# Performance work log

Measured on AMD Instinct MI355X. Metric: run time of the kernel, lower is better.

Reference implementation:

```python
import jax, jax.numpy as jnp
import numpy as np

N_NODES = 40000
N_EDGES = 640000
NFEAT = 256
NHID = 128


def setup_inputs() -> dict:
    key = jax.random.key(0)
    k1, k2, k3, k4 = jax.random.split(key, 4)
    x = jax.random.normal(k1, (N_NODES, NFEAT), dtype=jnp.float32)
    edge_index = jax.random.randint(k2, (2, N_EDGES), 0, N_NODES, dtype=jnp.int64)
    edge_weight = jax.random.uniform(k3, (N_EDGES,), dtype=jnp.float32)
    # Glorot-style init for the GraphConvolution weight, zero bias
    W = jax.random.normal(k4, (NFEAT, NHID), dtype=jnp.float32) * (1.0 / np.sqrt(NFEAT))
    b = jnp.zeros((NHID,), dtype=jnp.float32)
    return {"x": x, "edge_index": edge_index, "edge_weight": edge_weight, "W": W, "b": b}


def reference(x, edge_index, edge_weight, W, b):
    # GraphConvolution: support = x @ W ; out = spmm(adj, support) + b ; relu
    support = x @ W                                   # [N, nhid]
    src, dst = edge_index[0], edge_index[1]
    msgs = support[src] * edge_weight[:, None]        # [E, nhid] gathered messages
    agg = jax.ops.segment_sum(msgs, dst, num_segments=N_NODES)  # [N, nhid]
    return jax.nn.relu(agg + b)
```

## Files before the change

kernel.cpp:

```cpp
#include <hip/hip_runtime.h>

#define NNODES 40000
#define NEDGES 640000
#define NFEAT  256
#define NHID   128

#define RSHIFT 7
#define RNODES 128
#define NR     313
#define PARTB  250
#define EPT    10
#define EPB    2560
#define CAPB   32
#define GEMM_BLOCKS (NNODES / 64)
#define WSPLIT 4
#define WNODES 32
#define CAPW   1024

#define SUP_OFF  0u
#define WT_OFF   10240000u
#define CNT_OFF  10305536u
#define EBIN_OFF 10465536u
#define WS_NEEDED (EBIN_OFF + (size_t)NR * PARTB * CAPB * 8)

typedef float floatx4 __attribute__((ext_vector_type(4)));
typedef __bf16 bf16x8 __attribute__((ext_vector_type(8)));
typedef unsigned short ushort8 __attribute__((ext_vector_type(8)));
union BfFrag { ushort8 s; bf16x8 b; };

__device__ __forceinline__ unsigned short f2bf(float f) {
    unsigned int u = __float_as_uint(f);
    u = (u + 0x7FFFu + ((u >> 16) & 1u)) >> 16;
    return (unsigned short)u;
}

__device__ __forceinline__ float4 bf4(unsigned int lo, unsigned int hi) {
    float4 v;
    v.x = __uint_as_float(lo << 16);
    v.y = __uint_as_float(lo & 0xFFFF0000u);
    v.z = __uint_as_float(hi << 16);
    v.w = __uint_as_float(hi & 0xFFFF0000u);
    return v;
}

__global__ __launch_bounds__(256) void setup_wt(const float* __restrict__ W,
                                                unsigned short* __restrict__ Wt) {
    const int i = blockIdx.x * 256 + threadIdx.x;
    const int h = i >> 8;
    const int k = i & 255;
    Wt[i] = f2bf(W[k * NHID + h]);
}

__global__ __launch_bounds__(256) void gemm_fill(const float* __restrict__ x,
                                                 const unsigned short* __restrict__ Wt,
                                                 unsigned short* __restrict__ support,
                                                 const int* __restrict__ ei,
                                                 const float* __restrict__ ew,
                                                 unsigned short* __restrict__ cnt,
                                                 unsigned long long* __restrict__ ebin) {
    const int tid = threadIdx.x;

    if (blockIdx.x >= GEMM_BLOCKS) {
        __shared__ unsigned int ldscur[320];
        const int pb   = blockIdx.x - GEMM_BLOCKS;
        const int base = pb * EPB + tid;

        for (int i = tid; i < 320; i += 256) ldscur[i] = 0u;
        __syncthreads();

        int src[EPT], dst[EPT];
        float w[EPT];
        #pragma unroll
        for (int j = 0; j < EPT; j++) {
            const int e = base + j * 256;
            src[j] = ei[e];
            dst[j] = ei[NEDGES + e];
            w[j]   = ew[e];
        }
        #pragma unroll
        for (int j = 0; j < EPT; j++) {
            const int r = dst[j] >> RSHIFT;
            const unsigned int idx = atomicAdd(&ldscur[r], 1u);
            if (idx < CAPB) {
                const unsigned long long rec =
                    ((unsigned long long)f2bf(w[j]) << 32)
                  | ((unsigned long long)(dst[j] & (RNODES - 1)) << 16)
                  | (unsigned long long)(unsigned int)src[j];
                ebin[((size_t)r * PARTB + pb) * CAPB + idx] = rec;
            }
        }
        __syncthreads();

        for (int i = tid; i < NR; i += 256) {
            unsigned int c = ldscur[i];
            if (c > CAPB) c = CAPB;
            cnt[(size_t)pb * NR + i] = (unsigned short)c;
        }
        return;
    }

    const int lane = tid & 63;
    const int wv   = tid >> 6;
    const int m    = lane & 15;
    const int quad = lane >> 4;
    const int node = blockIdx.x * 64 + wv * 16 + m;

    BfFrag afrag[8];
    const float* xrow = x + (size_t)node * NFEAT + quad * 8;
    #pragma unroll
    for (int ks = 0; ks < 8; ks++) {
        float4 f0 = *(const float4*)(xrow + ks * 32);
        float4 f1 = *(const float4*)(xrow + ks * 32 + 4);
        afrag[ks].s[0] = f2bf(f0.x); afrag[ks].s[1] = f2bf(f0.y);
        afrag[ks].s[2] = f2bf(f0.z); afrag[ks].s[3] = f2bf(f0.w);
        afrag[ks].s[4] = f2bf(f1.x); afrag[ks].s[5] = f2bf(f1.y);
        afrag[ks].s[6] = f2bf(f1.z); afrag[ks].s[7] = f2bf(f1.w);
    }

    floatx4 acc[8];
    #pragma unroll
    for (int nt = 0; nt < 8; nt++) acc[nt] = (floatx4){0.f, 0.f, 0.f, 0.f};

    #pragma unroll
    for (int nt = 0; nt < 8; nt++) {
        const unsigned short* wrow = Wt + (size_t)(nt * 16 + m) * NFEAT + quad * 8;
        #pragma unroll
        for (int ks = 0; ks < 8; ks++) {
            BfFrag bfrag;
            bfrag.s = *(const ushort8*)(wrow + ks * 32);
            acc[nt] = __builtin_amdgcn_mfma_f32_16x16x32_bf16(afrag[ks].b, bfrag.b,
                                                              acc[nt], 0, 0, 0);
        }
    }

    const int row0 = blockIdx.x * 64 + wv * 16 + quad * 4;
    #pragma unroll
    for (int nt = 0; nt < 8; nt++) {
        #pragma unroll
        for (int r = 0; r < 4; r++) {
            support[(size_t)(row0 + r) * NHID + nt * 16 + m] = f2bf(acc[nt][r]);
        }
    }
}

__global__ __launch_bounds__(512) void gather_range(
        const unsigned short* __restrict__ cnt,
        const unsigned long long* __restrict__ ebin,
        const unsigned short* __restrict__ support,
        const float* __restrict__ b,
        float* __restrict__ out) {
    __shared__ unsigned long long srec[CAPW];
    __shared__ unsigned int hcnt[WNODES];
    __shared__ unsigned int hstart[WNODES + 1];
    __shared__ unsigned int sA[WNODES], sB[WNODES];

    const int r   = blockIdx.x >> 2;
    const int q   = blockIdx.x & 3;
    const int tid = threadIdx.x;

    unsigned int c_t = 0;
    const unsigned long long* seg =
        ebin + ((size_t)r * PARTB + (tid < PARTB ? tid : 0)) * CAPB;
    if (tid < PARTB) {
        c_t = cnt[(size_t)tid * NR + r];
        if (c_t > CAPB) c_t = CAPB;
    }
    if (tid < WNODES) hcnt[tid] = 0u;
    __syncthreads();

    for (unsigned int k = 0; k < c_t; ++k) {
        const unsigned int dl = (unsigned int)(seg[k] >> 16) & (RNODES - 1);
        if ((int)(dl >> 5) == q) atomicAdd(&hcnt[dl & (WNODES - 1)], 1u);
    }
    __syncthreads();

    if (tid < WNODES) sA[tid] = (tid > 0) ? hcnt[tid - 1] : 0u;
    __syncthreads();
    unsigned int* cur = sA;
    unsigned int* nxt = sB;
    for (int off = 1; off < WNODES; off <<= 1) {
        if (tid < WNODES) nxt[tid] = cur[tid] + ((tid >= off) ? cur[tid - off] : 0u);
        __syncthreads();
        unsigned int* t = cur; cur = nxt; nxt = t;
    }
    if (tid < WNODES) hstart[tid] = cur[tid];
    if (tid == WNODES - 1) hstart[WNODES] = cur[WNODES - 1] + hcnt[WNODES - 1];
    __syncthreads();
    if (tid < WNODES) hcnt[tid] = hstart[tid];
    __syncthreads();

    for (unsigned int k = 0; k < c_t; ++k) {
        const unsigned long long rec = seg[k];
        const unsigned int dl = (unsigned int)(rec >> 16) & (RNODES - 1);
        if ((int)(dl >> 5) == q) {
            const unsigned int p = atomicAdd(&hcnt[dl & (WNODES - 1)], 1u);
            if (p < CAPW) srec[p] = rec;
        }
    }
    __syncthreads();

    const int nl = tid >> 4;
    const int ql = tid & 15;
    unsigned int kb = hstart[nl];
    unsigned int ke = hstart[nl + 1];
    if (kb > CAPW) kb = CAPW;
    if (ke > CAPW) ke = CAPW;

    float4 lo = make_float4(0.f, 0.f, 0.f, 0.f);
    float4 hi = lo;
    const uint4* sup4 = (const uint4*)support;

    #pragma unroll 2
    for (unsigned int k = kb; k < ke; ++k) {
        const unsigned long long rec = srec[k];
        const float w  = __uint_as_float(((unsigned int)(rec >> 32)) << 16);
        const int   sc = (int)(rec & 0xFFFFu);
        const uint4 u  = sup4[(size_t)sc * 16 + ql];
        const float4 vl = bf4(u.x, u.y), vh = bf4(u.z, u.w);
        lo.x = fmaf(w, vl.x, lo.x); lo.y = fmaf(w, vl.y, lo.y);
        lo.z = fmaf(w, vl.z, lo.z); lo.w = fmaf(w, vl.w, lo.w);
        hi.x = fmaf(w, vh.x, hi.x); hi.y = fmaf(w, vh.y, hi.y);
        hi.z = fmaf(w, vh.z, hi.z); hi.w = fmaf(w, vh.w, hi.w);
    }

    const int node = r * RNODES + q * WNODES + nl;
    if (node < NNODES) {
        const float4* b4p = (const float4*)b;
        float4 bl = b4p[ql * 2], bh = b4p[ql * 2 + 1];
        lo.x = fmaxf(lo.x + bl.x, 0.f); lo.y = fmaxf(lo.y + bl.y, 0.f);
        lo.z = fmaxf(lo.z + bl.z, 0.f); lo.w = fmaxf(lo.w + bl.w, 0.f);
        hi.x = fmaxf(hi.x + bh.x, 0.f); hi.y = fmaxf(hi.y + bh.y, 0.f);
        hi.z = fmaxf(hi.z + bh.z, 0.f); hi.w = fmaxf(hi.w + bh.w, 0.f);
        float4* o4 = (float4*)out + (size_t)node * (NHID / 4);
        o4[ql * 2]     = lo;
        o4[ql * 2 + 1] = hi;
    }
}

__global__ __launch_bounds__(256) void gemm_xw(const float* __restrict__ x,
                                               const float* __restrict__ W,
                                               float* __restrict__ support) {
    __shared__ float xs[64 * NFEAT];
    const int tid   = threadIdx.x;
    const int node0 = blockIdx.x * 64;

    const float4* xg  = (const float4*)(x + (size_t)node0 * NFEAT);
    float4*       xs4 = (float4*)xs;
    #pragma unroll
    for (int i = tid; i < 64 * (NFEAT / 4); i += 256) xs4[i] = xg[i];
    __syncthreads();

    const int hg = tid & 31;
    const int ng = tid >> 5;
    const float4* W4 = (const float4*)W;

    float4 acc[8];
    #pragma unroll
    for (int n = 0; n < 8; n++) acc[n] = make_float4(0.f, 0.f, 0.f, 0.f);

    #pragma unroll 4
    for (int k = 0; k < NFEAT; k++) {
        float4 w = W4[k * (NHID / 4) + hg];
        #pragma unroll
        for (int n = 0; n < 8; n++) {
            float xv = xs[(ng * 8 + n) * NFEAT + k];
            acc[n].x = fmaf(xv, w.x, acc[n].x);
            acc[n].y = fmaf(xv, w.y, acc[n].y);
            acc[n].z = fmaf(xv, w.z, acc[n].z);
            acc[n].w = fmaf(xv, w.w, acc[n].w);
        }
    }

    float4* out4 = (float4*)support;
    #pragma unroll
    for (int n = 0; n < 8; n++)
        out4[(size_t)(node0 + ng * 8 + n) * (NHID / 4) + hg] = acc[n];
}

__global__ __launch_bounds__(256) void scatter_edges(const int* __restrict__ ei,
                                                     const float* __restrict__ ew,
                                                     const float* __restrict__ support,
                                                     float* __restrict__ out) {
    const int tid  = threadIdx.x;
    const int lane = tid & 31;
    const int e    = blockIdx.x * 8 + (tid >> 5);
    const int   src = ei[e];
    const int   dst = ei[NEDGES + e];
    const float w   = ew[e];
    const float4* s4 = (const float4*)support;
    float4 v = s4[(size_t)src * (NHID / 4) + lane];
    float* o = out + (size_t)dst * NHID + lane * 4;
    atomicAdd(o + 0, v.x * w);
    atomicAdd(o + 1, v.y * w);
    atomicAdd(o + 2, v.z * w);
    atomicAdd(o + 3, v.w * w);
}

__global__ __launch_bounds__(256) void finalize(float* __restrict__ out,
                                                const float* __restrict__ b) {
    const int i = blockIdx.x * 256 + threadIdx.x;
    float4*       o4 = (float4*)out;
    const float4* b4 = (const float4*)b;
    float4 v  = o4[i];
    float4 bb = b4[i & 31];
    v.x = fmaxf(v.x + bb.x, 0.f);
    v.y = fmaxf(v.y + bb.y, 0.f);
    v.z = fmaxf(v.z + bb.z, 0.f);
    v.w = fmaxf(v.w + bb.w, 0.f);
    o4[i] = v;
}

extern "C" void kernel_launch(void* const* d_in, const int* in_sizes, int n_in,
                              void* d_out, int out_size, void* d_ws, size_t ws_size,
                              hipStream_t stream) {
    const float* x  = (const float*)d_in[0];
    const int*   ei = (const int*)d_in[1];
    const float* ew = (const float*)d_in[2];
    const float* W  = (const float*)d_in[3];
    const float* b  = (const float*)d_in[4];
    float*       out = (float*)d_out;

    char* ws = (char*)d_ws;

    if (ws_size >= WS_NEEDED) {
        unsigned short*     support = (unsigned short*)(ws + SUP_OFF);
        unsigned short*     Wt      = (unsigned short*)(ws + WT_OFF);
        unsigned short*     cnt     = (unsigned short*)(ws + CNT_OFF);
        unsigned long long* ebin    = (unsigned long long*)(ws + EBIN_OFF);

        setup_wt<<<128, 256, 0, stream>>>(W, Wt);
        gemm_fill<<<GEMM_BLOCKS + PARTB, 256, 0, stream>>>(
            x, Wt, support, ei, ew, cnt, ebin);
        gather_range<<<NR * WSPLIT, 512, 0, stream>>>(cnt, ebin, support, b, out);
    } else {
        float* support = (float*)(ws + SUP_OFF);
        gemm_xw<<<NNODES / 64, 256, 0, stream>>>(x, W, support);
        hipMemsetAsync(d_out, 0, (size_t)out_size * sizeof(float), stream);
        scatter_edges<<<NEDGES / 8, 256, 0, stream>>>(ei, ew, support, out);
        finalize<<<out_size / 4 / 256, 256, 0, stream>>>(out, b);
    }
}
```

Measured before the change: 168.0 us.

## Bin edges directly into 32-node windows to avoid redundant bin scans

Edges are now binned per 32-node window (1250 bins, 16-slot capacity per partition block) instead of per 128-node range. Each gather block reads only its own window's records, so the four-fold redundant read and filter of every 128-node bin goes away. In exchange, the binning pass keeps more LDS counters, each partition gets a smaller per-bin cap, and the count array grows. Overflow is more likely at 16 slots (expected about 2 edges per bin per partition) but stays very unlikely.

```diff
diff --git a/kernel.cpp b/kernel.cpp
--- a/kernel.cpp
+++ b/kernel.cpp
@@ -5,23 +5,21 @@
 #define NFEAT  256
 #define NHID   128
 
-#define RSHIFT 7
-#define RNODES 128
-#define NR     313
+#define WSH    5
+#define WNODES 32
+#define NW     1250
 #define PARTB  250
 #define EPT    10
 #define EPB    2560
-#define CAPB   32
+#define CAPBW  16
+#define CAPW   1024
 #define GEMM_BLOCKS (NNODES / 64)
-#define WSPLIT 4
-#define WNODES 32
-#define CAPW   1024
 
 #define SUP_OFF  0u
 #define WT_OFF   10240000u
 #define CNT_OFF  10305536u
-#define EBIN_OFF 10465536u
-#define WS_NEEDED (EBIN_OFF + (size_t)NR * PARTB * CAPB * 8)
+#define EBIN_OFF 10930560u
+#define WS_NEEDED (EBIN_OFF + (size_t)NW * PARTB * CAPBW * 8)
 
 typedef float floatx4 __attribute__((ext_vector_type(4)));
 typedef __bf16 bf16x8 __attribute__((ext_vector_type(8)));
@@ -61,11 +59,11 @@
     const int tid = threadIdx.x;
 
     if (blockIdx.x >= GEMM_BLOCKS) {
-        __shared__ unsigned int ldscur[320];
+        __shared__ unsigned int ldscur[NW];
         const int pb   = blockIdx.x - GEMM_BLOCKS;
         const int base = pb * EPB + tid;
 
-        for (int i = tid; i < 320; i += 256) ldscur[i] = 0u;
+        for (int i = tid; i < NW; i += 256) ldscur[i] = 0u;
         __syncthreads();
 
         int src[EPT], dst[EPT];
@@ -79,22 +77,22 @@
         }
         #pragma unroll
         for (int j = 0; j < EPT; j++) {
-            const int r = dst[j] >> RSHIFT;
-            const unsigned int idx = atomicAdd(&ldscur[r], 1u);
-            if (idx < CAPB) {
+            const int rw = dst[j] >> WSH;
+            const unsigned int idx = atomicAdd(&ldscur[rw], 1u);
+            if (idx < CAPBW) {
                 const unsigned long long rec =
                     ((unsigned long long)f2bf(w[j]) << 32)
-                  | ((unsigned long long)(dst[j] & (RNODES - 1)) << 16)
+                  | ((unsigned long long)(dst[j] & (WNODES - 1)) << 16)
                   | (unsigned long long)(unsigned int)src[j];
-                ebin[((size_t)r * PARTB + pb) * CAPB + idx] = rec;
+                ebin[((size_t)rw * PARTB + pb) * CAPBW + idx] = rec;
             }
         }
         __syncthreads();
 
-        for (int i = tid; i < NR; i += 256) {
+        for (int i = tid; i < NW; i += 256) {
             unsigned int c = ldscur[i];
-            if (c > CAPB) c = CAPB;
-            cnt[(size_t)pb * NR + i] = (unsigned short)c;
+            if (c > CAPBW) c = CAPBW;
+            cnt[(size_t)pb * NW + i] = (unsigned short)c;
         }
         return;
     }
@@ -154,24 +152,21 @@
     __shared__ unsigned int hstart[WNODES + 1];
     __shared__ unsigned int sA[WNODES], sB[WNODES];
 
-    const int r   = blockIdx.x >> 2;
-    const int q   = blockIdx.x & 3;
+    const int rw  = blockIdx.x;
     const int tid = threadIdx.x;
 
     unsigned int c_t = 0;
     const unsigned long long* seg =
-        ebin + ((size_t)r * PARTB + (tid < PARTB ? tid : 0)) * CAPB;
+        ebin + ((size_t)rw * PARTB + (tid < PARTB ? tid : 0)) * CAPBW;
     if (tid < PARTB) {
-        c_t = cnt[(size_t)tid * NR + r];
-        if (c_t > CAPB) c_t = CAPB;
+        c_t = cnt[(size_t)tid * NW + rw];
+        if (c_t > CAPBW) c_t = CAPBW;
     }
     if (tid < WNODES) hcnt[tid] = 0u;
     __syncthreads();
 
-    for (unsigned int k = 0; k < c_t; ++k) {
-        const unsigned int dl = (unsigned int)(seg[k] >> 16) & (RNODES - 1);
-        if ((int)(dl >> 5) == q) atomicAdd(&hcnt[dl & (WNODES - 1)], 1u);
-    }
+    for (unsigned int k = 0; k < c_t; ++k)
+        atomicAdd(&hcnt[(unsigned int)(seg[k] >> 16) & (WNODES - 1)], 1u);
     __syncthreads();
 
     if (tid < WNODES) sA[tid] = (tid > 0) ? hcnt[tid - 1] : 0u;
@@ -191,11 +186,9 @@
 
     for (unsigned int k = 0; k < c_t; ++k) {
         const unsigned long long rec = seg[k];
-        const unsigned int dl = (unsigned int)(rec >> 16) & (RNODES - 1);
-        if ((int)(dl >> 5) == q) {
-            const unsigned int p = atomicAdd(&hcnt[dl & (WNODES - 1)], 1u);
-            if (p < CAPW) srec[p] = rec;
-        }
+        const unsigned int dl = (unsigned int)(rec >> 16) & (WNODES - 1);
+        const unsigned int p  = atomicAdd(&hcnt[dl], 1u);
+        if (p < CAPW) srec[p] = rec;
     }
     __syncthreads();
 
@@ -223,8 +216,8 @@
         hi.z = fmaf(w, vh.z, hi.z); hi.w = fmaf(w, vh.w, hi.w);
     }
 
-    const int node = r * RNODES + q * WNODES + nl;
-    if (node < NNODES) {
+    const int node = rw * WNODES + nl;
+    {
         const float4* b4p = (const float4*)b;
         float4 bl = b4p[ql * 2], bh = b4p[ql * 2 + 1];
         lo.x = fmaxf(lo.x + bl.x, 0.f); lo.y = fmaxf(lo.y + bl.y, 0.f);
@@ -331,7 +324,7 @@
         setup_wt<<<128, 256, 0, stream>>>(W, Wt);
         gemm_fill<<<GEMM_BLOCKS + PARTB, 256, 0, stream>>>(
             x, Wt, support, ei, ew, cnt, ebin);
-        gather_range<<<NR * WSPLIT, 512, 0, stream>>>(cnt, ebin, support, b, out);
+        gather_range<<<NW, 512, 0, stream>>>(cnt, ebin, support, b, out);
     } else {
         float* support = (float*)(ws + SUP_OFF);
         gemm_xw<<<NNODES / 64, 256, 0, stream>>>(x, W, support);
```

After: 155.6 us. -7.4%, faster.
